# Optimization experiments

Hardware: AMD Instinct MI355X
Metric: run time of the kernel (lower is better)

## Reference

```python
import jax, jax.numpy as jnp
import numpy as np

B_, L_, H_ = 8, 512, 768
DIN, N, R, K = 1536, 64, 48, 4  # d_inner, d_state, dt_rank, d_conv


def setup_inputs() -> dict:
    key = jax.random.key(0)
    ks = jax.random.split(key, 16)
    rn = lambda i, shp, sc=0.02: jax.random.normal(ks[i], shp, dtype=jnp.float32) * sc
    inp = {
        "text": jax.random.normal(ks[0], (B_, L_, H_), dtype=jnp.float32),
        "audio": jax.random.normal(ks[1], (B_, L_, H_), dtype=jnp.float32),
        "video": jax.random.normal(ks[2], (B_, L_, H_), dtype=jnp.float32),
        "proj_w": rn(3, (3 * H_, H_)),
        "proj_b": jnp.zeros((H_,), jnp.float32),
        "proj_ln_g": jnp.ones((H_,), jnp.float32),
        "proj_ln_b": jnp.zeros((H_,), jnp.float32),
        "blk_ln_g": jnp.ones((H_,), jnp.float32),
        "blk_ln_b": jnp.zeros((H_,), jnp.float32),
        "in_proj_w": rn(4, (H_, 2 * DIN)),
        "conv_w": rn(5, (DIN, 1, K), 0.1),
        "conv_b": jnp.zeros((DIN,), jnp.float32),
        "x_proj_w": rn(6, (DIN, R + 2 * N)),
        "dt_proj_w": rn(7, (R, DIN), 0.1),
        "dt_proj_b": jnp.full((DIN,), -4.6, jnp.float32),  # softplus -> ~0.01 dt
        "A_log": jnp.log(jnp.tile(jnp.arange(1, N + 1, dtype=jnp.float32), (DIN, 1))),
        "D": jnp.ones((DIN,), jnp.float32),
        "out_proj_w": rn(8, (DIN, H_)),
    }
    return inp


def _ln(x, g, b, eps=1e-5):
    mu = x.mean(-1, keepdims=True)
    xc = x - mu
    v = (xc * xc).mean(-1, keepdims=True)
    return xc * jax.lax.rsqrt(v + eps) * g + b


def _mamba(h, in_proj_w, conv_w, conv_b, x_proj_w, dt_proj_w, dt_proj_b, A_log, D, out_proj_w):
    Bsz, L, _ = h.shape
    xz = h @ in_proj_w                       # [B,L,2*DIN]
    x, z = jnp.split(xz, 2, axis=-1)         # each [B,L,DIN]
    # causal depthwise conv1d over time
    xc = jax.lax.conv_general_dilated(
        x.transpose(0, 2, 1), conv_w, (1,), [(K - 1, 0)],
        dimension_numbers=("NCH", "OIH", "NCH"), feature_group_count=DIN)
    x = jax.nn.silu(xc + conv_b[None, :, None]).transpose(0, 2, 1)  # [B,L,DIN]
    dbl = x @ x_proj_w                       # [B,L,R+2N]
    dt, Bm, Cm = jnp.split(dbl, [R, R + N], axis=-1)
    delta = jax.nn.softplus(dt @ dt_proj_w + dt_proj_b)  # [B,L,DIN]
    A = -jnp.exp(A_log)                      # [DIN,N]

    def step(hcar, t):
        d_t, b_t, c_t, u_t = t               # [B,DIN],[B,N],[B,N],[B,DIN]
        hcar = jnp.exp(d_t[..., None] * A) * hcar + (d_t * u_t)[..., None] * b_t[:, None, :]
        y = jnp.einsum("bdn,bn->bd", hcar, c_t)
        return hcar, y

    xs = (delta.transpose(1, 0, 2), Bm.transpose(1, 0, 2), Cm.transpose(1, 0, 2), x.transpose(1, 0, 2))
    h0 = jnp.zeros((Bsz, DIN, N), x.dtype)
    _, ys = jax.lax.scan(step, h0, xs)       # ys: [L,B,DIN]
    y = ys.transpose(1, 0, 2) + x * D
    y = y * jax.nn.silu(z)
    return y @ out_proj_w                    # [B,L,H]


def reference(text, audio, video, proj_w, proj_b, proj_ln_g, proj_ln_b,
              blk_ln_g, blk_ln_b, in_proj_w, conv_w, conv_b, x_proj_w,
              dt_proj_w, dt_proj_b, A_log, D, out_proj_w):
    fused = jnp.concatenate([text, audio, video], axis=-1) @ proj_w + proj_b
    fused = _ln(fused, proj_ln_g, proj_ln_b)
    m = _mamba(_ln(fused, blk_ln_g, blk_ln_b), in_proj_w, conv_w, conv_b,
               x_proj_w, dt_proj_w, dt_proj_b, A_log, D, out_proj_w)
    fused = fused + m                         # residual (dropout = identity in eval)
    return fused.mean(axis=1)                 # [B,H]
```

## Files before the change

### kernel.cpp

```cpp
#include <hip/hip_runtime.h>
#include <hip/hip_bf16.h>
#include <cstddef>
#include <cstdint>

#define DIN 1536
#define LSEQ 512

typedef __hip_bfloat16 bf16;
typedef __attribute__((ext_vector_type(8))) short short8x;
typedef __attribute__((ext_vector_type(4))) float f32x4;
typedef const __attribute__((address_space(1))) unsigned int* gp1;
typedef __attribute__((address_space(3))) unsigned int* lp3;

__device__ inline float readlane_f(float v, int l) {
  return __uint_as_float(__builtin_amdgcn_readlane(__float_as_uint(v), l));
}
__device__ inline void gload_lds(const bf16* g, unsigned short* l) {
  __builtin_amdgcn_global_load_lds((gp1)g, (lp3)l, 16, 0, 0);
}
__device__ inline void bsplit(float v, bf16& h, bf16& l) {
  h = __float2bfloat16(v);
  l = __float2bfloat16(v - __bfloat162float(h));
}
__device__ inline float softplusf(float t) {
  return fmaxf(t, 0.f) + log1pf(__expf(-fabsf(t)));
}
template<int CTRL>
__device__ inline float dpp_add(float v) {
  int t = __builtin_amdgcn_update_dpp(0, __float_as_int(v), CTRL, 0xf, 0xf, true);
  return v + __int_as_float(t);
}
__device__ inline float dpp_wave_sum(float p) {
  p = dpp_add<0x111>(p);
  p = dpp_add<0x112>(p);
  p = dpp_add<0x114>(p);
  p = dpp_add<0x118>(p);
  p = dpp_add<0x142>(p);
  p = dpp_add<0x143>(p);
  return p;
}

template<int TBM, int TBN, int WR, int WC, int AMODE, int EPI>
__global__ __launch_bounds__(WR*WC*64) void mgemm(
    const bf16* __restrict__ Ah0, const bf16* __restrict__ Al0,
    const bf16* __restrict__ Ah1, const bf16* __restrict__ Al1,
    const bf16* __restrict__ Ah2, const bf16* __restrict__ Al2,
    const bf16* __restrict__ Bh, const bf16* __restrict__ Bl,
    const float* __restrict__ bias,
    float* __restrict__ C, float* __restrict__ C2,
    bf16* __restrict__ Oh, bf16* __restrict__ Ol,
    int K, int lda, int ldc)
{
  constexpr int NW = WR * WC;
  constexpr int SM = TBM / WR, SN = TBN / WC;
  constexpr int T_M = SM / 16, T_N = SN / 16;
  __shared__ unsigned short sAh[TBM * 32], sAl[TBM * 32];
  __shared__ unsigned short sBh[TBN * 32], sBl[TBN * 32];
  const int tid = threadIdx.x;
  const int lane = tid & 63, wid = tid >> 6;
  const int bm = blockIdx.x * TBM, bn = blockIdx.y * TBN;
  const int wr = wid / WC, wc = wid % WC;

  const int stg_m = lane >> 2;
  const int stg_k = ((lane & 3) ^ ((lane >> 3) & 3)) * 8;
  const int fo = (lane & 15) * 64 + ((((lane >> 4) ^ ((lane >> 1) & 3)) & 3) * 16);

  f32x4 acc[T_M][T_N];
  #pragma unroll
  for (int i = 0; i < T_M; ++i)
    #pragma unroll
    for (int j = 0; j < T_N; ++j) acc[i][j] = (f32x4){0.f, 0.f, 0.f, 0.f};

  for (int k0 = 0; k0 < K; k0 += 32) {
    __syncthreads();
    const bf16* pAh; const bf16* pAl; int ka;
    if (AMODE == 1) {
      int seg = k0 / 768;
      pAh = (seg == 0) ? Ah0 : (seg == 1) ? Ah1 : Ah2;
      pAl = (seg == 0) ? Al0 : (seg == 1) ? Al1 : Al2;
      ka = k0 - seg * 768;
    } else { pAh = Ah0; pAl = Al0; ka = k0; }
    #pragma unroll
    for (int q = wid; q < TBM / 16; q += NW) {
      size_t go = (size_t)(bm + q * 16 + stg_m) * lda + ka + stg_k;
      gload_lds(pAh + go, &sAh[q * 512]);
      gload_lds(pAl + go, &sAl[q * 512]);
    }
    #pragma unroll
    for (int q = wid; q < TBN / 16; q += NW) {
      size_t go = (size_t)(bn + q * 16 + stg_m) * K + k0 + stg_k;
      gload_lds(Bh + go, &sBh[q * 512]);
      gload_lds(Bl + go, &sBl[q * 512]);
    }
    __syncthreads();

    short8x ah[T_M], al[T_M], bh[T_N], bl[T_N];
    #pragma unroll
    for (int mi = 0; mi < T_M; ++mi) {
      int off = (wr * SM + mi * 16) * 64 + fo;
      ah[mi] = *(const short8x*)((const char*)sAh + off);
      al[mi] = *(const short8x*)((const char*)sAl + off);
    }
    #pragma unroll
    for (int nj = 0; nj < T_N; ++nj) {
      int off = (wc * SN + nj * 16) * 64 + fo;
      bh[nj] = *(const short8x*)((const char*)sBh + off);
      bl[nj] = *(const short8x*)((const char*)sBl + off);
    }
    #pragma unroll
    for (int mi = 0; mi < T_M; ++mi)
      #pragma unroll
      for (int nj = 0; nj < T_N; ++nj) {
        acc[mi][nj] = __builtin_amdgcn_mfma_f32_16x16x32_bf16(ah[mi], bh[nj], acc[mi][nj], 0, 0, 0);
        acc[mi][nj] = __builtin_amdgcn_mfma_f32_16x16x32_bf16(ah[mi], bl[nj], acc[mi][nj], 0, 0, 0);
        acc[mi][nj] = __builtin_amdgcn_mfma_f32_16x16x32_bf16(al[mi], bh[nj], acc[mi][nj], 0, 0, 0);
      }
  }

  const int cl = lane & 15, qd = lane >> 4;
  const int colbase = bn + wc * SN;
  const int rowbase = bm + wr * SM;
  if (EPI == 1) {
    #pragma unroll
    for (int mi = 0; mi < T_M; ++mi) {
      int r0 = rowbase + mi * 16 + qd * 4;
      #pragma unroll
      for (int nj = 0; nj < T_N; ++nj) {
        int col = colbase + nj * 16 + cl;
        float bv = bias[col];
        #pragma unroll
        for (int rg = 0; rg < 4; ++rg)
          C[(size_t)(r0 + rg) * ldc + col] = acc[mi][nj][rg] + bv;
      }
    }
  } else if (EPI == 4) {
    #pragma unroll
    for (int mi = 0; mi < T_M; ++mi) {
      int m = rowbase + mi * 16 + qd * 4;
      int b = m >> 9, l = m & 511;
      #pragma unroll
      for (int nj = 0; nj < T_N; ++nj) {
        int col = colbase + nj * 16 + cl;
        float bv = bias[col];
        float4 v;
        v.x = softplusf(acc[mi][nj][0] + bv);
        v.y = softplusf(acc[mi][nj][1] + bv);
        v.z = softplusf(acc[mi][nj][2] + bv);
        v.w = softplusf(acc[mi][nj][3] + bv);
        *reinterpret_cast<float4*>(&C[((size_t)b * DIN + col) * LSEQ + l]) = v;
      }
    }
  } else if (EPI == 5) {
    if (bn < 1536) {
      #pragma unroll
      for (int mi = 0; mi < T_M; ++mi) {
        int r0 = rowbase + mi * 16 + qd * 4;
        #pragma unroll
        for (int nj = 0; nj < T_N; ++nj) {
          int col = colbase + nj * 16 + cl;
          #pragma unroll
          for (int rg = 0; rg < 4; ++rg)
            C[(size_t)(r0 + rg) * ldc + col] = acc[mi][nj][rg];
        }
      }
    } else {
      #pragma unroll
      for (int mi = 0; mi < T_M; ++mi) {
        int m = rowbase + mi * 16 + qd * 4;
        int b = m >> 9, l = m & 511;
        #pragma unroll
        for (int nj = 0; nj < T_N; ++nj) {
          int colz = colbase - 1536 + nj * 16 + cl;
          float4 v;
          v.x = acc[mi][nj][0]; v.y = acc[mi][nj][1];
          v.z = acc[mi][nj][2]; v.w = acc[mi][nj][3];
          *reinterpret_cast<float4*>(&C2[((size_t)b * DIN + colz) * LSEQ + l]) = v;
        }
      }
    }
  } else if (EPI == 6) {
    #pragma unroll
    for (int mi = 0; mi < T_M; ++mi) {
      int r0 = rowbase + mi * 16 + qd * 4;
      #pragma unroll
      for (int nj = 0; nj < T_N; ++nj) {
        int col = colbase + nj * 16 + cl;
        #pragma unroll
        for (int rg = 0; rg < 4; ++rg) {
          float v = acc[mi][nj][rg];
          C[(size_t)(r0 + rg) * 192 + col] = v;
          if (col < 64) {
            bf16 h, l;
            if (col < 48) bsplit(v, h, l);
            else { h = __float2bfloat16(0.f); l = h; }
            Oh[(size_t)(r0 + rg) * 64 + col] = h;
            Ol[(size_t)(r0 + rg) * 64 + col] = l;
          }
        }
      }
    }
  }
}

__global__ __launch_bounds__(256) void prep_k(
    const float* __restrict__ s0, const float* __restrict__ s1,
    const float* __restrict__ s2, bf16* __restrict__ moddst,
    const float* __restrict__ pw, const float* __restrict__ ipw,
    const float* __restrict__ xpw, const float* __restrict__ dtw,
    bf16* pwTh, bf16* pwTl, bf16* ipTh, bf16* ipTl,
    bf16* xpTh, bf16* xpTl, bf16* dtTh, bf16* dtTl)
{
  __shared__ float T[64][65];
  const int tid = threadIdx.x;
  if (blockIdx.x < 36864) {
    const int per = 4096 * 768 / 256;
    int seg = blockIdx.x / per;
    int idx = (blockIdx.x - seg * per) * 256 + tid;
    const float* src = (seg == 0) ? s0 : (seg == 1) ? s1 : s2;
    bf16* hi = moddst + (size_t)seg * 2 * 4096 * 768;
    bf16* lo = hi + (size_t)4096 * 768;
    bf16 h, l; bsplit(src[idx], h, l);
    hi[idx] = h; lo[idx] = l;
    return;
  }
  const int id = blockIdx.x - 36864;
  const float* src; bf16 *hi, *lo; int P, Q, ld, Ppad, px, qx;
  if (id < 432)       { src = pw;  hi = pwTh; lo = pwTl; P = 2304; Q = 768;  ld = 768;  Ppad = 2304; px = id % 36;          qx = id / 36; }
  else if (id < 1008) { int i = id - 432;  src = ipw; hi = ipTh; lo = ipTl; P = 768;  Q = 3072; ld = 3072; Ppad = 768;  px = i % 12; qx = i / 12; }
  else if (id < 1080) { int i = id - 1008; src = xpw; hi = xpTh; lo = xpTl; P = 1536; Q = 176;  ld = 176;  Ppad = 1536; px = i % 24; qx = i / 24; }
  else                { int i = id - 1080; src = dtw; hi = dtTh; lo = dtTl; P = 48;   Q = 1536; ld = 1536; Ppad = 64;   px = 0;      qx = i; }
  const int p0 = px * 64, q0 = qx * 64;
  {
    int j = tid & 63, i0 = tid >> 6;
    for (int i = i0; i < 64; i += 4) {
      int p = p0 + i, q = q0 + j;
      T[i][j] = (p < P && q < Q) ? src[(size_t)p * ld + q] : 0.f;
    }
  }
  __syncthreads();
  {
    int ii = tid & 63, j0 = tid >> 6;
    for (int jj = j0; jj < 64; jj += 4) {
      bf16 h, l; bsplit(T[ii][jj], h, l);
      size_t o = (size_t)(q0 + jj) * Ppad + p0 + ii;
      hi[o] = h; lo[o] = l;
    }
  }
}

__device__ inline float block_sum256(float s, float* red) {
  #pragma unroll
  for (int o = 32; o > 0; o >>= 1) s += __shfl_xor(s, o, 64);
  int tid = threadIdx.x;
  __syncthreads();
  if ((tid & 63) == 0) red[tid >> 6] = s;
  __syncthreads();
  return red[0] + red[1] + red[2] + red[3];
}

__global__ __launch_bounds__(256) void ln2_k(
    const float* __restrict__ pre,
    const float* __restrict__ g1, const float* __restrict__ b1,
    const float* __restrict__ g2, const float* __restrict__ b2,
    float* __restrict__ fused, bf16* __restrict__ hAh, bf16* __restrict__ hAl)
{
  __shared__ float red[4];
  const int row = blockIdx.x;
  const int tid = threadIdx.x;
  const float* x = pre + (size_t)row * 768;
  float v0 = x[tid], v1 = x[tid + 256], v2 = x[tid + 512];

  float mu = block_sum256(v0 + v1 + v2, red) * (1.f / 768.f);
  float c0 = v0 - mu, c1 = v1 - mu, c2 = v2 - mu;
  float var = block_sum256(c0*c0 + c1*c1 + c2*c2, red) * (1.f / 768.f);
  float r = rsqrtf(var + 1e-5f);
  float f0 = c0 * r * g1[tid] + b1[tid];
  float f1 = c1 * r * g1[tid + 256] + b1[tid + 256];
  float f2 = c2 * r * g1[tid + 512] + b1[tid + 512];
  float* fo = fused + (size_t)row * 768;
  fo[tid] = f0; fo[tid + 256] = f1; fo[tid + 512] = f2;

  float mu2 = block_sum256(f0 + f1 + f2, red) * (1.f / 768.f);
  float d0 = f0 - mu2, d1 = f1 - mu2, d2 = f2 - mu2;
  float var2 = block_sum256(d0*d0 + d1*d1 + d2*d2, red) * (1.f / 768.f);
  float r2 = rsqrtf(var2 + 1e-5f);
  float h0 = d0 * r2 * g2[tid] + b2[tid];
  float h1 = d1 * r2 * g2[tid + 256] + b2[tid + 256];
  float h2 = d2 * r2 * g2[tid + 512] + b2[tid + 512];
  bf16 hh, hl;
  size_t o = (size_t)row * 768;
  bsplit(h0, hh, hl); hAh[o + tid] = hh; hAl[o + tid] = hl;
  bsplit(h1, hh, hl); hAh[o + tid + 256] = hh; hAl[o + tid + 256] = hl;
  bsplit(h2, hh, hl); hAh[o + tid + 512] = hh; hAl[o + tid + 512] = hl;
}

__global__ __launch_bounds__(256) void conv2x_k(
    const float* __restrict__ xbuf, const float* __restrict__ w,
    const float* __restrict__ cb, float* __restrict__ xct,
    bf16* __restrict__ xcAh, bf16* __restrict__ xcAl)
{
  __shared__ float Xs[67][65];
  __shared__ float Ys[64][65];
  const int tid = threadIdx.x;
  const int l0 = blockIdx.x * 64;
  const int d0 = blockIdx.y * 64;
  const int b  = blockIdx.z;
  for (int e = tid; e < 67 * 64; e += 256) {
    int r = e >> 6, dd = e & 63;
    int l = l0 - 3 + r;
    Xs[r][dd] = (l >= 0) ? xbuf[((size_t)b * 512 + l) * DIN + d0 + dd] : 0.f;
  }
  __syncthreads();
  {
    const int lane = tid & 63, grp = tid >> 6;
    #pragma unroll
    for (int i = 0; i < 16; ++i) {
      int dd = grp + i * 4;
      int d = d0 + dd;
      float acc = cb[d];
      #pragma unroll
      for (int k = 0; k < 4; ++k)
        acc = fmaf(Xs[lane + k][dd], w[d * 4 + k], acc);
      float v = acc / (1.f + __expf(-acc));
      xct[((size_t)b * DIN + d) * LSEQ + l0 + lane] = v;
      Ys[lane][dd] = v;
    }
  }
  __syncthreads();
  {
    const int dd = tid & 63, lg = tid >> 6;
    #pragma unroll
    for (int j = 0; j < 16; ++j) {
      int l = lg * 16 + j;
      bf16 h, lo; bsplit(Ys[l][dd], h, lo);
      size_t o = (size_t)(b * 512 + l0 + l) * DIN + d0 + dd;
      xcAh[o] = h; xcAl[o] = lo;
    }
  }
}

__global__ __launch_bounds__(512) void scan6_k(
    const float* __restrict__ delta_t, const float* __restrict__ xct,
    const float* __restrict__ dbl, const float* __restrict__ zt,
    const float* __restrict__ A_log, const float* __restrict__ Dv,
    float* __restrict__ ysbar)
{
  __shared__ float BC[64][128];
  const int tid = threadIdx.x;
  const int lane = tid & 63;
  const int wv = tid >> 6;
  const int bid = blockIdx.x;
  const int b = bid / 192;
  const int d = (bid - b * 192) * 8 + wv;
  const float Ad2 = -__expf(A_log[d * 64 + lane]) * 1.442695041f;
  const float Dd = Dv[d];
  const size_t strm = ((size_t)b * DIN + d) * LSEQ;
  float h = 0.f;
  float a = 0.f;
  float us = 0.f;

  for (int l0 = 0; l0 < LSEQ; l0 += 64) {
    __syncthreads();
    #pragma unroll
    for (int i = 0; i < 8; ++i) {
      int t = wv * 8 + i;
      const float* src = dbl + (size_t)(b * LSEQ + l0 + t) * 192;
      float2 v; v.x = src[48 + lane]; v.y = src[112 + lane];
      *reinterpret_cast<float2*>(&BC[t][lane * 2]) = v;
    }
    float dt_v = delta_t[strm + l0 + lane];
    float u_v  = xct[strm + l0 + lane];
    float z_v  = zt[strm + l0 + lane];
    float du_v = dt_v * u_v;
    float sz_v = z_v / (1.f + __expf(-z_v));
    us += u_v * sz_v;
    __syncthreads();

    #pragma unroll
    for (int t = 0; t < 64; ++t) {
      float sdt = readlane_f(dt_v, t);
      float sdu = readlane_f(du_v, t);
      float ssz = readlane_f(sz_v, t);
      float2 bc = *reinterpret_cast<const float2*>(&BC[t][lane * 2]);
      float e = exp2f(sdt * Ad2);
      h = fmaf(e, h, sdu * bc.x);
      a = fmaf(h, bc.y * ssz, a);
    }
  }
  float tot = readlane_f(dpp_wave_sum(a + Dd * us), 63);
  if (lane == 0) ysbar[b * 1536 + d] = tot;
}

__global__ __launch_bounds__(256) void final2_k(
    const float* __restrict__ fused, const float* __restrict__ ysbar,
    const float* __restrict__ W, float* __restrict__ out)
{
  const int c = blockIdx.x * 256 + threadIdx.x;
  const int b = blockIdx.y;
  const int s = blockIdx.z;
  float part = 0.f;
  if (s < 8) {
    const int l0 = s * 64;
    const float* fp = fused + (size_t)((b << 9) + l0) * 768 + c;
    #pragma unroll 4
    for (int l = 0; l < 64; ++l) part += fp[(size_t)l * 768];
  } else {
    const int d0 = (s - 8) * 96;
    #pragma unroll 4
    for (int i = 0; i < 96; ++i) {
      int d = d0 + i;
      part = fmaf(ysbar[b * 1536 + d], W[(size_t)d * 768 + c], part);
    }
  }
  atomicAdd(&out[b * 768 + c], part * (1.f / 512.f));
}

extern "C" void kernel_launch(void* const* d_in, const int* in_sizes, int n_in,
                              void* d_out, int out_size, void* d_ws, size_t ws_size,
                              hipStream_t stream)
{
  const float* text      = (const float*)d_in[0];
  const float* audio     = (const float*)d_in[1];
  const float* video     = (const float*)d_in[2];
  const float* proj_w    = (const float*)d_in[3];
  const float* proj_b    = (const float*)d_in[4];
  const float* proj_ln_g = (const float*)d_in[5];
  const float* proj_ln_b = (const float*)d_in[6];
  const float* blk_ln_g  = (const float*)d_in[7];
  const float* blk_ln_b  = (const float*)d_in[8];
  const float* in_proj_w = (const float*)d_in[9];
  const float* conv_w    = (const float*)d_in[10];
  const float* conv_b    = (const float*)d_in[11];
  const float* x_proj_w  = (const float*)d_in[12];
  const float* dt_proj_w = (const float*)d_in[13];
  const float* dt_proj_b = (const float*)d_in[14];
  const float* A_log     = (const float*)d_in[15];
  const float* Dv        = (const float*)d_in[16];
  const float* out_projw = (const float*)d_in[17];
  float* out = (float*)d_out;

  char* p = (char*)d_ws;
  const size_t P768 = (size_t)4096 * 768 * 2;
  char* S1 = p; p += 6 * P768;
  char* SW = p; p += 18087936;
  char* S3 = p; p += (size_t)4096 * 768 * 4;
  char* S4 = p; p += (size_t)4096 * 768 * 4;
  char* S6 = p; p += (size_t)4096 * 1536 * 4;
  char* S7 = p; p += (size_t)4096 * 1536 * 4;
  char* S8 = p; p += (size_t)4096 * 1536 * 4;
  char* SD = p; p += (size_t)4096 * 64 * 4;
  char* S9 = p; p += (size_t)4096 * 192 * 4;
  char* SY = p; p += 12288 * 4;

  bf16* modspl = (bf16*)S1;
  bf16 *tAh = (bf16*)S1,              *tAl = (bf16*)(S1 + P768);
  bf16 *aAh = (bf16*)(S1 + 2 * P768), *aAl = (bf16*)(S1 + 3 * P768);
  bf16 *vAh = (bf16*)(S1 + 4 * P768), *vAl = (bf16*)(S1 + 5 * P768);
  bf16 *hAh = (bf16*)S1,              *hAl = (bf16*)(S1 + P768);
  bf16 *xcAh = (bf16*)S1,             *xcAl = (bf16*)(S1 + (size_t)4096 * 1536 * 2);
  bf16 *pwTh = (bf16*)SW,                    *pwTl = pwTh + (size_t)768 * 2304;
  bf16 *ipTh = pwTl + (size_t)768 * 2304,    *ipTl = ipTh + (size_t)3072 * 768;
  bf16 *xpTh = ipTl + (size_t)3072 * 768,    *xpTl = xpTh + (size_t)192 * 1536;
  bf16 *dtTh = xpTl + (size_t)192 * 1536,    *dtTl = dtTh + (size_t)1536 * 64;
  float* pre     = (float*)S3;
  float* fused   = (float*)S4;
  float* xbuf    = (float*)S6;  float* delta_t = (float*)S6;
  float* zt      = (float*)S7;
  float* xct     = (float*)S8;
  bf16 *dtAh = (bf16*)SD, *dtAl = (bf16*)(SD + (size_t)4096 * 64 * 2);
  float* dbl     = (float*)S9;
  float* ysbar   = (float*)SY;

  prep_k<<<37968, 256, 0, stream>>>(text, audio, video, modspl,
                                    proj_w, in_proj_w, x_proj_w, dt_proj_w,
                                    pwTh, pwTl, ipTh, ipTl, xpTh, xpTl, dtTh, dtTl);
  mgemm<128, 128, 2, 2, 1, 1><<<dim3(32, 6), 256, 0, stream>>>(
      tAh, tAl, aAh, aAl, vAh, vAl, pwTh, pwTl, proj_b,
      pre, nullptr, nullptr, nullptr, 2304, 768, 768);
  ln2_k<<<4096, 256, 0, stream>>>(pre, proj_ln_g, proj_ln_b, blk_ln_g, blk_ln_b, fused, hAh, hAl);
  mgemm<128, 128, 2, 2, 0, 5><<<dim3(32, 24), 256, 0, stream>>>(
      hAh, hAl, nullptr, nullptr, nullptr, nullptr, ipTh, ipTl, nullptr,
      xbuf, zt, nullptr, nullptr, 768, 768, 1536);
  conv2x_k<<<dim3(8, 24, 8), 256, 0, stream>>>(xbuf, conv_w, conv_b, xct, xcAh, xcAl);
  mgemm<64, 64, 4, 2, 0, 6><<<dim3(64, 3), 512, 0, stream>>>(
      xcAh, xcAl, nullptr, nullptr, nullptr, nullptr, xpTh, xpTl, nullptr,
      dbl, nullptr, dtAh, dtAl, 1536, 1536, 192);
  mgemm<128, 128, 2, 2, 0, 4><<<dim3(32, 12), 256, 0, stream>>>(
      dtAh, dtAl, nullptr, nullptr, nullptr, nullptr, dtTh, dtTl, dt_proj_b,
      delta_t, nullptr, nullptr, nullptr, 64, 64, 0);
  scan6_k<<<1536, 512, 0, stream>>>(delta_t, xct, dbl, zt, A_log, Dv, ysbar);
  hipMemsetAsync(d_out, 0, (size_t)out_size * sizeof(float), stream);
  final2_k<<<dim3(3, 8, 24), 256, 0, stream>>>(fused, ysbar, out_projw, out);
}
```

Measured before the change: 568.9 us.

## Precompute delta*u and silu(z) in GEMM epilogues; scan reads scalar streams

The in_proj GEMM epilogue now applies silu to z before storing it, and the dt_proj epilogue also writes delta*u into a reuse of the S1 scratch buffer. The scan kernel then loads dt, du and silu(z) through wave-uniform pointers as scalar loads in batches of 16, replacing the per-step readlane broadcasts. This aims to shorten the serial scan inner loop and drop the exp work there, at the cost of an extra 4096x1536 fp32 write plus read. S1 is free at that point because xcAh/xcAl are already consumed by the x_proj GEMM.

```diff
diff --git a/kernel.cpp b/kernel.cpp
--- a/kernel.cpp
+++ b/kernel.cpp
@@ -39,6 +39,12 @@
   p = dpp_add<0x143>(p);
   return p;
 }
+__device__ inline const float* uniform_ptr(const float* p) {
+  unsigned long long v = (unsigned long long)p;
+  unsigned lo = __builtin_amdgcn_readfirstlane((unsigned)v);
+  unsigned hi = __builtin_amdgcn_readfirstlane((unsigned)(v >> 32));
+  return (const float*)(((unsigned long long)hi << 32) | lo);
+}
 
 template<int TBM, int TBN, int WR, int WC, int AMODE, int EPI>
 __global__ __launch_bounds__(WR*WC*64) void mgemm(
@@ -46,7 +52,7 @@
     const bf16* __restrict__ Ah1, const bf16* __restrict__ Al1,
     const bf16* __restrict__ Ah2, const bf16* __restrict__ Al2,
     const bf16* __restrict__ Bh, const bf16* __restrict__ Bl,
-    const float* __restrict__ bias,
+    const float* __restrict__ bias, const float* __restrict__ xin,
     float* __restrict__ C, float* __restrict__ C2,
     bf16* __restrict__ Oh, bf16* __restrict__ Ol,
     int K, int lda, int ldc)
@@ -142,12 +148,17 @@
       for (int nj = 0; nj < T_N; ++nj) {
         int col = colbase + nj * 16 + cl;
         float bv = bias[col];
+        size_t idx = ((size_t)b * DIN + col) * LSEQ + l;
         float4 v;
         v.x = softplusf(acc[mi][nj][0] + bv);
         v.y = softplusf(acc[mi][nj][1] + bv);
         v.z = softplusf(acc[mi][nj][2] + bv);
         v.w = softplusf(acc[mi][nj][3] + bv);
-        *reinterpret_cast<float4*>(&C[((size_t)b * DIN + col) * LSEQ + l]) = v;
+        *reinterpret_cast<float4*>(&C[idx]) = v;
+        const float4 xw = *reinterpret_cast<const float4*>(&xin[idx]);
+        float4 w;
+        w.x = v.x * xw.x; w.y = v.y * xw.y; w.z = v.z * xw.z; w.w = v.w * xw.w;
+        *reinterpret_cast<float4*>(&C2[idx]) = w;
       }
     }
   } else if (EPI == 5) {
@@ -172,8 +183,11 @@
         for (int nj = 0; nj < T_N; ++nj) {
           int colz = colbase - 1536 + nj * 16 + cl;
           float4 v;
-          v.x = acc[mi][nj][0]; v.y = acc[mi][nj][1];
-          v.z = acc[mi][nj][2]; v.w = acc[mi][nj][3];
+          #pragma unroll
+          for (int rg = 0; rg < 4; ++rg) {
+            float z = acc[mi][nj][rg];
+            ((float*)&v)[rg] = z / (1.f + __expf(-z));
+          }
           *reinterpret_cast<float4*>(&C2[((size_t)b * DIN + colz) * LSEQ + l]) = v;
         }
       }
@@ -339,9 +353,10 @@
   }
 }
 
-__global__ __launch_bounds__(512) void scan6_k(
-    const float* __restrict__ delta_t, const float* __restrict__ xct,
-    const float* __restrict__ dbl, const float* __restrict__ zt,
+__global__ __launch_bounds__(512) void scan8_k(
+    const float* __restrict__ delta_t, const float* __restrict__ dut,
+    const float* __restrict__ szt, const float* __restrict__ xct,
+    const float* __restrict__ dbl,
     const float* __restrict__ A_log, const float* __restrict__ Dv,
     float* __restrict__ ysbar)
 {
@@ -355,6 +370,9 @@
   const float Ad2 = -__expf(A_log[d * 64 + lane]) * 1.442695041f;
   const float Dd = Dv[d];
   const size_t strm = ((size_t)b * DIN + d) * LSEQ;
+  const float* pdt = uniform_ptr(delta_t + strm);
+  const float* pdu = uniform_ptr(dut + strm);
+  const float* psz = uniform_ptr(szt + strm);
   float h = 0.f;
   float a = 0.f;
   float us = 0.f;
@@ -368,23 +386,31 @@
       float2 v; v.x = src[48 + lane]; v.y = src[112 + lane];
       *reinterpret_cast<float2*>(&BC[t][lane * 2]) = v;
     }
-    float dt_v = delta_t[strm + l0 + lane];
-    float u_v  = xct[strm + l0 + lane];
-    float z_v  = zt[strm + l0 + lane];
-    float du_v = dt_v * u_v;
-    float sz_v = z_v / (1.f + __expf(-z_v));
-    us += u_v * sz_v;
+    {
+      float u_v  = xct[strm + l0 + lane];
+      float sz_v = szt[strm + l0 + lane];
+      us = fmaf(u_v, sz_v, us);
+    }
     __syncthreads();
 
     #pragma unroll
-    for (int t = 0; t < 64; ++t) {
-      float sdt = readlane_f(dt_v, t);
-      float sdu = readlane_f(du_v, t);
-      float ssz = readlane_f(sz_v, t);
-      float2 bc = *reinterpret_cast<const float2*>(&BC[t][lane * 2]);
-      float e = exp2f(sdt * Ad2);
-      h = fmaf(e, h, sdu * bc.x);
-      a = fmaf(h, bc.y * ssz, a);
+    for (int sub = 0; sub < 4; ++sub) {
+      float sdt[16], sdu[16], ssz[16];
+      #pragma unroll
+      for (int i = 0; i < 16; ++i) {
+        int t = l0 + sub * 16 + i;
+        sdt[i] = pdt[t];
+        sdu[i] = pdu[t];
+        ssz[i] = psz[t];
+      }
+      #pragma unroll
+      for (int i = 0; i < 16; ++i) {
+        int t = sub * 16 + i;
+        float2 bc = *reinterpret_cast<const float2*>(&BC[t][lane * 2]);
+        float e = exp2f(sdt[i] * Ad2);
+        h = fmaf(e, h, sdu[i] * bc.x);
+        a = fmaf(h, bc.y * ssz[i], a);
+      }
     }
   }
   float tot = readlane_f(dpp_wave_sum(a + Dd * us), 63);
@@ -458,6 +484,7 @@
   bf16 *vAh = (bf16*)(S1 + 4 * P768), *vAl = (bf16*)(S1 + 5 * P768);
   bf16 *hAh = (bf16*)S1,              *hAl = (bf16*)(S1 + P768);
   bf16 *xcAh = (bf16*)S1,             *xcAl = (bf16*)(S1 + (size_t)4096 * 1536 * 2);
+  float* dut = (float*)S1;
   bf16 *pwTh = (bf16*)SW,                    *pwTl = pwTh + (size_t)768 * 2304;
   bf16 *ipTh = pwTl + (size_t)768 * 2304,    *ipTl = ipTh + (size_t)3072 * 768;
   bf16 *xpTh = ipTl + (size_t)3072 * 768,    *xpTl = xpTh + (size_t)192 * 1536;
@@ -465,7 +492,7 @@
   float* pre     = (float*)S3;
   float* fused   = (float*)S4;
   float* xbuf    = (float*)S6;  float* delta_t = (float*)S6;
-  float* zt      = (float*)S7;
+  float* szt     = (float*)S7;
   float* xct     = (float*)S8;
   bf16 *dtAh = (bf16*)SD, *dtAl = (bf16*)(SD + (size_t)4096 * 64 * 2);
   float* dbl     = (float*)S9;
@@ -475,20 +502,20 @@
                                     proj_w, in_proj_w, x_proj_w, dt_proj_w,
                                     pwTh, pwTl, ipTh, ipTl, xpTh, xpTl, dtTh, dtTl);
   mgemm<128, 128, 2, 2, 1, 1><<<dim3(32, 6), 256, 0, stream>>>(
-      tAh, tAl, aAh, aAl, vAh, vAl, pwTh, pwTl, proj_b,
+      tAh, tAl, aAh, aAl, vAh, vAl, pwTh, pwTl, proj_b, nullptr,
       pre, nullptr, nullptr, nullptr, 2304, 768, 768);
   ln2_k<<<4096, 256, 0, stream>>>(pre, proj_ln_g, proj_ln_b, blk_ln_g, blk_ln_b, fused, hAh, hAl);
   mgemm<128, 128, 2, 2, 0, 5><<<dim3(32, 24), 256, 0, stream>>>(
-      hAh, hAl, nullptr, nullptr, nullptr, nullptr, ipTh, ipTl, nullptr,
-      xbuf, zt, nullptr, nullptr, 768, 768, 1536);
+      hAh, hAl, nullptr, nullptr, nullptr, nullptr, ipTh, ipTl, nullptr, nullptr,
+      xbuf, szt, nullptr, nullptr, 768, 768, 1536);
   conv2x_k<<<dim3(8, 24, 8), 256, 0, stream>>>(xbuf, conv_w, conv_b, xct, xcAh, xcAl);
   mgemm<64, 64, 4, 2, 0, 6><<<dim3(64, 3), 512, 0, stream>>>(
-      xcAh, xcAl, nullptr, nullptr, nullptr, nullptr, xpTh, xpTl, nullptr,
+      xcAh, xcAl, nullptr, nullptr, nullptr, nullptr, xpTh, xpTl, nullptr, nullptr,
       dbl, nullptr, dtAh, dtAl, 1536, 1536, 192);
   mgemm<128, 128, 2, 2, 0, 4><<<dim3(32, 12), 256, 0, stream>>>(
-      dtAh, dtAl, nullptr, nullptr, nullptr, nullptr, dtTh, dtTl, dt_proj_b,
-      delta_t, nullptr, nullptr, nullptr, 64, 64, 0);
-  scan6_k<<<1536, 512, 0, stream>>>(delta_t, xct, dbl, zt, A_log, Dv, ysbar);
+      dtAh, dtAl, nullptr, nullptr, nullptr, nullptr, dtTh, dtTl, dt_proj_b, xct,
+      delta_t, dut, nullptr, nullptr, 64, 64, 0);
+  scan8_k<<<1536, 512, 0, stream>>>(delta_t, dut, szt, xct, dbl, A_log, Dv, ysbar);
   hipMemsetAsync(d_out, 0, (size_t)out_size * sizeof(float), stream);
   final2_k<<<dim3(3, 8, 24), 256, 0, stream>>>(fused, ysbar, out_projw, out);
 }
```

Result: slower. 621.8 us (+9.3%).
